# Kernel optimization log

Measured on AMD Instinct MI355X. Metric: run time of the kernel, lower is better.

Reference implementation:

```python
import jax, jax.numpy as jnp
import numpy as np

HW = 256  # fixed UV/image resolution hardcoded in the module


def _grid_sample_nearest(inp, grid):
    """torch.F.grid_sample(mode='nearest', padding_mode='zeros', align_corners=False).
    inp: [N,C,H,W], grid: [N,Hg,Wg,2] with (x,y) in [-1,1]. Returns [N,C,Hg,Wg]."""
    N, C, H, W = inp.shape
    x = grid[..., 0]
    y = grid[..., 1]
    # align_corners=False pixel mapping
    ix = jnp.round(((x + 1.0) * W - 1.0) * 0.5).astype(jnp.int32)
    iy = jnp.round(((y + 1.0) * H - 1.0) * 0.5).astype(jnp.int32)
    valid = (ix >= 0) & (ix < W) & (iy >= 0) & (iy < H)
    ixc = jnp.clip(ix, 0, W - 1)
    iyc = jnp.clip(iy, 0, H - 1)
    gathered = jax.vmap(lambda im, yy, xx: im[:, yy, xx])(inp, iyc, ixc)  # [N,C,Hg,Wg]
    return gathered * valid[:, None, :, :].astype(inp.dtype)


def setup_inputs() -> dict:
    key = jax.random.key(0)
    k1, k2, k3, k4 = jax.random.split(key, 4)
    bs = 128
    grid = jax.random.uniform(k1, (bs, 2, HW, HW), jnp.float32, -1.0, 1.0)
    seg = jax.random.uniform(k2, (bs, 1, HW, HW), jnp.float32)
    conf_is = jax.random.uniform(k3, (bs, 1, HW, HW), jnp.float32)
    depth = jax.random.normal(k4, (bs, 1, HW, HW), jnp.float32)
    return {"grid": grid, "seg": seg, "conf_is": conf_is, "depth": depth}


def reference(grid, seg, conf_is, depth):
    bs = grid.shape[0]
    # segmentation mask with all-True fallback for empty masks
    seg_mask = seg > 0.5  # [bs,1,H,W] bool
    n_valid = jnp.sum(seg_mask, axis=(1, 2, 3))
    seg_mask = jnp.where((n_valid == 0)[:, None, None, None], True, seg_mask)

    gridm = grid * seg_mask  # bool broadcast over channel dim
    grid_int = ((gridm + 1.0) * 0.5 * HW).astype(jnp.int32)  # trunc-toward-zero == torch .long()
    grid_int = jnp.clip(grid_int, 0, HW - 1)

    # meshgrid_uv[h, w] = [w, h]
    hh, ww = jnp.meshgrid(jnp.arange(HW), jnp.arange(HW), indexing='ij')
    mesh_uv = jnp.stack([ww, hh], axis=-1).astype(jnp.float32)  # [H,W,2]

    # per-batch scatter write: grid_uv[b, gy, gx] = mesh_uv  (the irregular-access hot spot)
    def scatter_one(gy, gx):
        return jnp.zeros((HW, HW, 2), jnp.float32).at[gy, gx].set(mesh_uv)

    grid_uv = jax.vmap(scatter_one)(grid_int[:, 1], grid_int[:, 0])  # [bs,H,W,2]
    grid_uv = grid_uv / 128.0 - 1.0

    mesh_x = jnp.broadcast_to((ww / 280.0).astype(jnp.float32)[None, None], (bs, 1, HW, HW))
    mesh_y = jnp.broadcast_to((hh / 280.0).astype(jnp.float32)[None, None], (bs, 1, HW, HW))
    dkpt_img = jnp.concatenate([mesh_x, mesh_y, depth], axis=1) * seg_mask  # [bs,3,H,W]

    dkpt_uv = _grid_sample_nearest(dkpt_img, grid_uv)           # [bs,3,H,W]
    conf_is_uv = _grid_sample_nearest(conf_is, grid_uv)          # [bs,1,H,W]
    mask_uv = _grid_sample_nearest(seg_mask.astype(jnp.float32), grid_uv)[:, 0]  # [bs,H,W]
    return dkpt_uv, conf_is_uv, mask_uv
```

## Files before the change

kernel.cpp:

```cpp
#include <hip/hip_runtime.h>

#define HW    256
#define HW2   65536
#define BS    128
#define NT    1024
#define QPB   16384
#define HQ    8192

__device__ __forceinline__ void lds_max_u16(unsigned int* W32, int cell, unsigned int val) {
    unsigned int* word = W32 + (cell >> 1);
    unsigned int sh = (cell & 1) << 4;
    unsigned int assumed = *word;
    while (((assumed >> sh) & 0xFFFFu) < val) {
        unsigned int nw = (assumed & ~(0xFFFFu << sh)) | (val << sh);
        unsigned int prev = atomicCAS(word, assumed, nw);
        if (prev == assumed) break;
        assumed = prev;
    }
}

__global__ __launch_bounds__(NT, 1) void fused_kernel(
        const float* __restrict__ grid,
        const float* __restrict__ seg,
        const float* __restrict__ conf,
        const float* __restrict__ depth,
        float* __restrict__ out) {
    __shared__ unsigned short Wl[HW2];
    __shared__ unsigned long long segbits[4][256];
    __shared__ int red[16];
    __shared__ int flag_s;

    const int b    = blockIdx.x >> 1;
    const int half = blockIdx.x & 1;
    const int tid  = threadIdx.x;
    const int wave = tid >> 6;
    const int lane = tid & 63;
    unsigned int* W32 = (unsigned int*)Wl;

    const float* segb   = seg   + (size_t)b * HW2;
    const float* confb  = conf  + (size_t)b * HW2;
    const float* depthb = depth + (size_t)b * HW2;

    {
        uint4* Wz = (uint4*)W32;
        #pragma unroll
        for (int k = 0; k < 8; ++k) Wz[tid + k * NT] = make_uint4(0u, 0u, 0u, 0u);
    }
    unsigned long long mbits = 0ULL;
    int cnt = 0;
    {
        const float4* s4 = (const float4*)segb;
        #pragma unroll
        for (int k = 0; k < 16; ++k) {
            int i = tid + k * NT;
            float4 v = s4[i];
            bool px = v.x > 0.5f, py = v.y > 0.5f, pz = v.z > 0.5f, pw = v.w > 0.5f;
            unsigned long long bx = __ballot(px);
            unsigned long long by = __ballot(py);
            unsigned long long bz = __ballot(pz);
            unsigned long long bw = __ballot(pw);
            if (lane == 0) {
                int wi = wave + k * 16;
                segbits[0][wi] = bx; segbits[1][wi] = by;
                segbits[2][wi] = bz; segbits[3][wi] = bw;
                cnt += __popcll(bx) + __popcll(by) + __popcll(bz) + __popcll(bw);
            }
            unsigned long long q = (px ? 1ULL : 0ULL) | (py ? 2ULL : 0ULL) |
                                   (pz ? 4ULL : 0ULL) | (pw ? 8ULL : 0ULL);
            mbits |= q << (k * 4);
        }
    }
    if (lane == 0) red[wave] = cnt;
    __syncthreads();
    if (tid == 0) {
        int t = 0;
        #pragma unroll
        for (int w = 0; w < 16; ++w) t += red[w];
        flag_s = (t == 0) ? 1 : 0;
    }
    __syncthreads();
    const int flagb = flag_s;

    {
        const float4* gx4 = (const float4*)(grid + (size_t)(2 * b) * HW2);
        const float4* gy4 = (const float4*)(grid + (size_t)(2 * b + 1) * HW2);
        int masked_max = -1;
        #pragma unroll 4
        for (int k = 0; k < 16; ++k) {
            int i = tid + k * NT;
            float4 X = gx4[i];
            float4 Y = gy4[i];
            int hw0 = i * 4;
            float xa[4] = {X.x, X.y, X.z, X.w};
            float ya[4] = {Y.x, Y.y, Y.z, Y.w};
            #pragma unroll
            for (int j = 0; j < 4; ++j) {
                bool m = flagb || ((mbits >> (k * 4 + j)) & 1ULL);
                if (m) {
                    float fx = (xa[j] + 1.0f) * 0.5f * 256.0f;
                    float fy = (ya[j] + 1.0f) * 0.5f * 256.0f;
                    int gxi = min(max((int)fx, 0), HW - 1);
                    int gyi = min(max((int)fy, 0), HW - 1);
                    lds_max_u16(W32, gyi * HW + gxi, (unsigned int)(hw0 + j));
                } else {
                    masked_max = hw0 + j;
                }
            }
        }
        int mm = masked_max;
        for (int off = 32; off > 0; off >>= 1) mm = max(mm, __shfl_xor(mm, off));
        if (lane == 0 && mm >= 0)
            lds_max_u16(W32, 128 * HW + 128, (unsigned int)mm);
    }
    __syncthreads();

    float4* out4 = (float4*)out;
    const size_t dkBase = (size_t)(b * 3) * QPB;
    const size_t O1q = (size_t)BS * 3 * QPB + (size_t)b * QPB;
    const size_t O2q = (size_t)BS * 4 * QPB + (size_t)b * QPB;
    #pragma unroll 4
    for (int k = 0; k < 8; ++k) {
        int i = half * HQ + tid + k * NT;
        uint2 wv = *(const uint2*)(Wl + 4 * i);
        unsigned la[4] = {wv.x & 0xFFFFu, wv.x >> 16, wv.y & 0xFFFFu, wv.y >> 16};
        float o0[4], o1[4], o2[4], oc[4], om[4];
        #pragma unroll
        for (int j = 0; j < 4; ++j) {
            unsigned l = la[j];
            int ix = (int)(l & 255u) & ~1;
            int iy = (int)(l >> 8) & ~1;
            int off = iy * HW + ix;
            int q = off >> 2;
            float m;
            if (flagb) m = 1.0f;
            else       m = (float)((segbits[off & 3][q >> 6] >> (q & 63)) & 1ULL);
            o0[j] = ((float)ix / 280.0f) * m;
            o1[j] = ((float)iy / 280.0f) * m;
            o2[j] = depthb[off] * m;
            oc[j] = confb[off];
            om[j] = m;
        }
        out4[dkBase + i]           = make_float4(o0[0], o0[1], o0[2], o0[3]);
        out4[dkBase + QPB + i]     = make_float4(o1[0], o1[1], o1[2], o1[3]);
        out4[dkBase + 2 * QPB + i] = make_float4(o2[0], o2[1], o2[2], o2[3]);
        out4[O1q + i]              = make_float4(oc[0], oc[1], oc[2], oc[3]);
        out4[O2q + i]              = make_float4(om[0], om[1], om[2], om[3]);
    }
}

extern "C" void kernel_launch(void* const* d_in, const int* in_sizes, int n_in,
                              void* d_out, int out_size, void* d_ws, size_t ws_size,
                              hipStream_t stream) {
    const float* grid  = (const float*)d_in[0];
    const float* seg   = (const float*)d_in[1];
    const float* conf  = (const float*)d_in[2];
    const float* depth = (const float*)d_in[3];
    float* out = (float*)d_out;
    fused_kernel<<<BS * 2, NT, 0, stream>>>(grid, seg, conf, depth, out);
}
```

Baseline: 353.0 us.

## Split scatter table by row half and use native 32-bit LDS atomicMax

Each block now builds only its half of the 256x256 winner table (rows 0-127 or 128-255) in 32-bit shared words. This replaces the emulated 16-bit CAS-loop max with the hardware LDS atomicMax and skips scatter writes that land in the other half. The block-to-batch mapping is also changed so the two halves of a batch sit in different launch groups. Each block still reads the full grid and seg for its batch, so input reads stay duplicated.

```diff
diff --git a/kernel.cpp b/kernel.cpp
--- a/kernel.cpp
+++ b/kernel.cpp
@@ -7,42 +7,29 @@
 #define QPB   16384
 #define HQ    8192
 
-__device__ __forceinline__ void lds_max_u16(unsigned int* W32, int cell, unsigned int val) {
-    unsigned int* word = W32 + (cell >> 1);
-    unsigned int sh = (cell & 1) << 4;
-    unsigned int assumed = *word;
-    while (((assumed >> sh) & 0xFFFFu) < val) {
-        unsigned int nw = (assumed & ~(0xFFFFu << sh)) | (val << sh);
-        unsigned int prev = atomicCAS(word, assumed, nw);
-        if (prev == assumed) break;
-        assumed = prev;
-    }
-}
-
 __global__ __launch_bounds__(NT, 1) void fused_kernel(
         const float* __restrict__ grid,
         const float* __restrict__ seg,
         const float* __restrict__ conf,
         const float* __restrict__ depth,
         float* __restrict__ out) {
-    __shared__ unsigned short Wl[HW2];
+    __shared__ unsigned int Wl[HW2 / 2];
     __shared__ unsigned long long segbits[4][256];
     __shared__ int red[16];
     __shared__ int flag_s;
 
-    const int b    = blockIdx.x >> 1;
-    const int half = blockIdx.x & 1;
+    const int b    = blockIdx.x & (BS - 1);
+    const int half = blockIdx.x >> 7;
     const int tid  = threadIdx.x;
     const int wave = tid >> 6;
     const int lane = tid & 63;
-    unsigned int* W32 = (unsigned int*)Wl;
 
     const float* segb   = seg   + (size_t)b * HW2;
     const float* confb  = conf  + (size_t)b * HW2;
     const float* depthb = depth + (size_t)b * HW2;
 
     {
-        uint4* Wz = (uint4*)W32;
+        uint4* Wz = (uint4*)Wl;
         #pragma unroll
         for (int k = 0; k < 8; ++k) Wz[tid + k * NT] = make_uint4(0u, 0u, 0u, 0u);
     }
@@ -101,7 +88,8 @@
                     float fy = (ya[j] + 1.0f) * 0.5f * 256.0f;
                     int gxi = min(max((int)fx, 0), HW - 1);
                     int gyi = min(max((int)fy, 0), HW - 1);
-                    lds_max_u16(W32, gyi * HW + gxi, (unsigned int)(hw0 + j));
+                    if ((gyi >> 7) == half)
+                        atomicMax(&Wl[(gyi & 127) * HW + gxi], (unsigned int)(hw0 + j));
                 } else {
                     masked_max = hw0 + j;
                 }
@@ -109,8 +97,8 @@
         }
         int mm = masked_max;
         for (int off = 32; off > 0; off >>= 1) mm = max(mm, __shfl_xor(mm, off));
-        if (lane == 0 && mm >= 0)
-            lds_max_u16(W32, 128 * HW + 128, (unsigned int)mm);
+        if (half == 1 && lane == 0 && mm >= 0)
+            atomicMax(&Wl[(128 & 127) * HW + 128], (unsigned int)mm);
     }
     __syncthreads();
 
@@ -120,9 +108,9 @@
     const size_t O2q = (size_t)BS * 4 * QPB + (size_t)b * QPB;
     #pragma unroll 4
     for (int k = 0; k < 8; ++k) {
-        int i = half * HQ + tid + k * NT;
-        uint2 wv = *(const uint2*)(Wl + 4 * i);
-        unsigned la[4] = {wv.x & 0xFFFFu, wv.x >> 16, wv.y & 0xFFFFu, wv.y >> 16};
+        int i = tid + k * NT;
+        uint4 wv = ((const uint4*)Wl)[i];
+        unsigned la[4] = {wv.x, wv.y, wv.z, wv.w};
         float o0[4], o1[4], o2[4], oc[4], om[4];
         #pragma unroll
         for (int j = 0; j < 4; ++j) {
@@ -140,11 +128,12 @@
             oc[j] = confb[off];
             om[j] = m;
         }
-        out4[dkBase + i]           = make_float4(o0[0], o0[1], o0[2], o0[3]);
-        out4[dkBase + QPB + i]     = make_float4(o1[0], o1[1], o1[2], o1[3]);
-        out4[dkBase + 2 * QPB + i] = make_float4(o2[0], o2[1], o2[2], o2[3]);
-        out4[O1q + i]              = make_float4(oc[0], oc[1], oc[2], oc[3]);
-        out4[O2q + i]              = make_float4(om[0], om[1], om[2], om[3]);
+        size_t gq = (size_t)half * HQ + i;
+        out4[dkBase + gq]           = make_float4(o0[0], o0[1], o0[2], o0[3]);
+        out4[dkBase + QPB + gq]     = make_float4(o1[0], o1[1], o1[2], o1[3]);
+        out4[dkBase + 2 * QPB + gq] = make_float4(o2[0], o2[1], o2[2], o2[3]);
+        out4[O1q + gq]              = make_float4(oc[0], oc[1], oc[2], oc[3]);
+        out4[O2q + gq]              = make_float4(om[0], om[1], om[2], om[3]);
     }
 }
 
```

Result: faster. 343.6 us (-2.7%).
